# Kernel tuning notes

Hardware: AMD Instinct MI355X
Metric: run time of the kernel (lower is better)

The kernel has to match this reference:

```python
import jax, jax.numpy as jnp
import numpy as np

N_NODES = 100000
N_EDGES = 1600000
NODES_PER_GRAPH = 100  # equal-sized graphs -> batch = arange // 100
POOL_K = 30


def setup_inputs() -> dict:
    key = jax.random.key(0)
    ks = jax.random.split(key, 8)
    F_IN, H1, H2, OUT = 128, 128, 128, 64
    x = jax.random.normal(ks[0], (N_NODES, F_IN), dtype=jnp.float32)
    edge_index = jax.random.randint(ks[1], (2, N_EDGES), 0, N_NODES, dtype=jnp.int64)
    batch = (jnp.arange(N_NODES, dtype=jnp.int64) // NODES_PER_GRAPH)
    # Glorot-ish init for weights, zero bias (as PyG GCNConv defaults)
    W1 = jax.random.normal(ks[2], (F_IN, H1), dtype=jnp.float32) / np.sqrt(F_IN)
    b1 = jnp.zeros((H1,), dtype=jnp.float32)
    W2 = jax.random.normal(ks[3], (H1, H2), dtype=jnp.float32) / np.sqrt(H1)
    b2 = jnp.zeros((H2,), dtype=jnp.float32)
    W3 = jax.random.normal(ks[4], (H2, OUT), dtype=jnp.float32) / np.sqrt(H2)
    b3 = jnp.zeros((OUT,), dtype=jnp.float32)
    return {"x": x, "edge_index": edge_index, "batch": batch,
            "W1": W1, "b1": b1, "W2": W2, "b2": b2, "W3": W3, "b3": b3}


def _gcn_conv(x, src, dst, W, b):
    """PyG GCNConv: xW, add self-loops, symmetric D^-1/2 A D^-1/2 scatter-add, +bias."""
    n = x.shape[0]
    loops = jnp.arange(n, dtype=src.dtype)
    row = jnp.concatenate([src, loops])  # message source
    col = jnp.concatenate([dst, loops])  # aggregation target
    xw = x @ W
    deg = jax.ops.segment_sum(jnp.ones(col.shape[0], x.dtype), col, num_segments=n)
    dinv = jnp.where(deg > 0, jax.lax.rsqrt(deg), 0.0)
    norm = dinv[row] * dinv[col]  # [E+N]
    out = jax.ops.segment_sum(xw[row] * norm[:, None], col, num_segments=n)
    return out + b


def _sort_pool(x, k):
    """global_sort_pool: per-graph descending sort by last channel, take top-k, flatten.
    Graphs are equal-sized and contiguous, so reshape to [B, P, C]."""
    n, c = x.shape
    xb = x.reshape(n // NODES_PER_GRAPH, NODES_PER_GRAPH, c)  # [B, P, C]
    order = jnp.argsort(-xb[..., -1], axis=1)[:, :k]          # [B, k]
    topk = jnp.take_along_axis(xb, order[..., None], axis=1)  # [B, k, C]
    return topk.reshape(topk.shape[0], k * c)


def reference(x, edge_index, batch, W1, b1, W2, b2, W3, b3):
    src, dst = edge_index[0], edge_index[1]
    h = jax.nn.relu(_gcn_conv(x, src, dst, W1, b1))
    h = jax.nn.relu(_gcn_conv(h, src, dst, W2, b2))
    h = _gcn_conv(h, src, dst, W3, b3)
    return _sort_pool(h, POOL_K)
```

## Files before the change

kernel.cpp:

```cpp
#include <hip/hip_runtime.h>
#include <math.h>

static inline size_t ws_align(size_t x) { return (x + 255) & ~(size_t)255; }

__global__ void count_kernel(const int* __restrict__ dst, int* __restrict__ counts, int E) {
  int e = blockIdx.x * 256 + threadIdx.x;
  if (e < E) atomicAdd(&counts[dst[e]], 1);
}

__global__ __launch_bounds__(256) void scanA_kernel(const int* __restrict__ counts,
    int* __restrict__ bsums, int n) {
  __shared__ int red[4];
  const int base = blockIdx.x * 1024;
  const int tid = threadIdx.x;
  int s = 0;
  #pragma unroll
  for (int u = 0; u < 4; ++u) {
    int i = base + u * 256 + tid;
    s += (i < n) ? counts[i] : 0;
  }
  #pragma unroll
  for (int m = 1; m < 64; m <<= 1) s += __shfl_xor(s, m, 64);
  if ((tid & 63) == 0) red[tid >> 6] = s;
  __syncthreads();
  if (tid == 0) bsums[blockIdx.x] = red[0] + red[1] + red[2] + red[3];
}

__global__ __launch_bounds__(128) void scanB_kernel(int* __restrict__ bsums, int nb) {
  __shared__ int tmp[129];
  int tid = threadIdx.x;
  tmp[tid] = (tid < nb) ? bsums[tid] : 0;
  __syncthreads();
  if (tid == 0) {
    int run = 0;
    for (int i = 0; i < nb; ++i) { int v = tmp[i]; tmp[i] = run; run += v; }
  }
  __syncthreads();
  if (tid < nb) bsums[tid] = tmp[tid];
}

__global__ __launch_bounds__(1024) void scanC_kernel(const int* __restrict__ counts,
    const int* __restrict__ bsums, int* __restrict__ offsets, int* __restrict__ cursor,
    double* __restrict__ dinv, int n) {
  __shared__ int warpsums[16];
  const int tid = threadIdx.x;
  const int lane = tid & 63, wid = tid >> 6;
  const int i = blockIdx.x * 1024 + tid;
  int v = (i < n) ? counts[i] : 0;
  int x = v;
  #pragma unroll
  for (int d = 1; d < 64; d <<= 1) {
    int y = __shfl_up(x, d, 64);
    if (lane >= d) x += y;
  }
  if (lane == 63) warpsums[wid] = x;
  __syncthreads();
  if (wid == 0) {
    int w = (lane < 16) ? warpsums[lane] : 0;
    #pragma unroll
    for (int d = 1; d < 16; d <<= 1) {
      int y = __shfl_up(w, d, 64);
      if (lane >= d) w += y;
    }
    if (lane < 16) warpsums[lane] = w;
  }
  __syncthreads();
  int excl = bsums[blockIdx.x] + x - v + (wid > 0 ? warpsums[wid - 1] : 0);
  if (i < n) {
    offsets[i] = excl;
    cursor[i] = excl;
    dinv[i] = 1.0 / sqrt((double)(v + 1));
    if (i == n - 1) offsets[n] = excl + v;
  }
}

__global__ void scatter_kernel(const int* __restrict__ src, const int* __restrict__ dst,
    int* __restrict__ cursor, int* __restrict__ srcs, float* __restrict__ ew,
    const double* __restrict__ dinv, int E, int use_ew) {
  int e = blockIdx.x * 256 + threadIdx.x;
  if (e < E) {
    int s = src[e], d = dst[e];
    int p = atomicAdd(&cursor[d], 1);
    srcs[p] = s;
    if (use_ew) ew[p] = (float)(dinv[s] * dinv[d]);
  }
}

template<int H>
__global__ __launch_bounds__(512, 4) void gemm_kernel(const float* __restrict__ X,
    const float* __restrict__ W, float* __restrict__ out, int N) {
  __shared__ float xs[128 * 68];
  const int tid  = threadIdx.x;
  const int row0 = blockIdx.x * 64;
  #pragma unroll
  for (int p = 0; p < 4; ++p) {
    int idx = p * 512 + tid;
    int r  = idx & 63;
    int c4 = idx >> 6;
    int grow = row0 + r;
    float4 v = make_float4(0.f, 0.f, 0.f, 0.f);
    if (grow < N) v = *(const float4*)(X + (size_t)grow * 128 + c4 * 4);
    float vals[4] = {v.x, v.y, v.z, v.w};
    #pragma unroll
    for (int j = 0; j < 4; ++j)
      xs[(4 * c4 + j) * 68 + r] = vals[j];
  }
  __syncthreads();
  constexpr int CPT = H / 32;
  const int rowg = tid & 15;
  const int colg = tid >> 4;
  const float* wbase = W + colg * CPT;

  double acc[4][CPT];
  #pragma unroll
  for (int j = 0; j < 4; ++j)
    #pragma unroll
    for (int h = 0; h < CPT; ++h) acc[j][h] = 0.0;

  float4 aA = *(const float4*)(xs + 4 * rowg);
  float4 aB;
  float bA[CPT], bB[CPT];
  #pragma unroll
  for (int h = 0; h < CPT; ++h) bA[h] = wbase[h];

  #pragma unroll 1
  for (int k = 0; k < 128; k += 2) {
    aB = *(const float4*)(xs + (k + 1) * 68 + 4 * rowg);
    #pragma unroll
    for (int h = 0; h < CPT; ++h) bB[h] = wbase[(size_t)(k + 1) * H + h];
    {
      double a0 = (double)aA.x, a1 = (double)aA.y, a2 = (double)aA.z, a3 = (double)aA.w;
      double b[CPT];
      #pragma unroll
      for (int h = 0; h < CPT; ++h) b[h] = (double)bA[h];
      #pragma unroll
      for (int h = 0; h < CPT; ++h) {
        acc[0][h] = fma(a0, b[h], acc[0][h]);
        acc[1][h] = fma(a1, b[h], acc[1][h]);
        acc[2][h] = fma(a2, b[h], acc[2][h]);
        acc[3][h] = fma(a3, b[h], acc[3][h]);
      }
    }
    if (k + 2 < 128) {
      aA = *(const float4*)(xs + (k + 2) * 68 + 4 * rowg);
      #pragma unroll
      for (int h = 0; h < CPT; ++h) bA[h] = wbase[(size_t)(k + 2) * H + h];
    }
    {
      double a0 = (double)aB.x, a1 = (double)aB.y, a2 = (double)aB.z, a3 = (double)aB.w;
      double b[CPT];
      #pragma unroll
      for (int h = 0; h < CPT; ++h) b[h] = (double)bB[h];
      #pragma unroll
      for (int h = 0; h < CPT; ++h) {
        acc[0][h] = fma(a0, b[h], acc[0][h]);
        acc[1][h] = fma(a1, b[h], acc[1][h]);
        acc[2][h] = fma(a2, b[h], acc[2][h]);
        acc[3][h] = fma(a3, b[h], acc[3][h]);
      }
    }
  }
  #pragma unroll
  for (int j = 0; j < 4; ++j) {
    int grow = row0 + rowg * 4 + j;
    if (grow < N) {
      float* o = out + (size_t)grow * H + colg * CPT;
      if constexpr (CPT == 4) {
        float4 v = make_float4((float)acc[j][0], (float)acc[j][1],
                               (float)acc[j][2], (float)acc[j][3]);
        *(float4*)o = v;
      } else {
        float2 v = make_float2((float)acc[j][0], (float)acc[j][1]);
        *(float2*)o = v;
      }
    }
  }
}

template<int C, bool RELU, bool USE_EW>
__global__ __launch_bounds__(256) void gather_kernel(const float* __restrict__ xw,
    const double* __restrict__ dinv, const int* __restrict__ offs,
    const int* __restrict__ srcs, const float* __restrict__ ew,
    const float* __restrict__ bias, float* __restrict__ out, int N) {
  constexpr int LPR = C / 4;
  constexpr int EPI = 64 / LPR;
  constexpr int U = 8;
  const int node = blockIdx.x * 4 + (threadIdx.x >> 6);
  if (node >= N) return;
  const int lane = threadIdx.x & 63;
  const int grp  = lane / LPR;
  const int c0   = (lane % LPR) * 4;
  const int e0 = offs[node], e1 = offs[node + 1];
  const double di = dinv[node];
  double a0 = 0.0, a1 = 0.0, a2 = 0.0, a3 = 0.0;

  for (int base = e0; base < e1; base += U * EPI) {
    int ss[U];
    double ww[U];
    float4 vv[U];
    #pragma unroll
    for (int u = 0; u < U; ++u) {
      int ee = base + u * EPI + grp;
      int cl = ee < e1 ? ee : e1 - 1;
      ss[u] = srcs[cl];
      if (USE_EW) ww[u] = (double)ew[cl];
    }
    #pragma unroll
    for (int u = 0; u < U; ++u) {
      vv[u] = *(const float4*)(xw + (size_t)ss[u] * C + c0);
      if (!USE_EW) ww[u] = dinv[ss[u]];
    }
    #pragma unroll
    for (int u = 0; u < U; ++u) {
      int ee = base + u * EPI + grp;
      double w = (ee < e1) ? ww[u] : 0.0;
      a0 = fma(w, (double)vv[u].x, a0);
      a1 = fma(w, (double)vv[u].y, a1);
      a2 = fma(w, (double)vv[u].z, a2);
      a3 = fma(w, (double)vv[u].w, a3);
    }
  }
  #pragma unroll
  for (int m = LPR; m < 64; m <<= 1) {
    a0 += __shfl_xor(a0, m, 64);
    a1 += __shfl_xor(a1, m, 64);
    a2 += __shfl_xor(a2, m, 64);
    a3 += __shfl_xor(a3, m, 64);
  }
  if (grp == 0) {
    const double d2 = di * di;
    float4 sv = *(const float4*)(xw + (size_t)node * C + c0);
    float4 bv = *(const float4*)(bias + c0);
    double o0, o1, o2, o3;
    if (USE_EW) {
      o0 = a0 + fma(d2, (double)sv.x, (double)bv.x);
      o1 = a1 + fma(d2, (double)sv.y, (double)bv.y);
      o2 = a2 + fma(d2, (double)sv.z, (double)bv.z);
      o3 = a3 + fma(d2, (double)sv.w, (double)bv.w);
    } else {
      o0 = fma(di, a0, fma(d2, (double)sv.x, (double)bv.x));
      o1 = fma(di, a1, fma(d2, (double)sv.y, (double)bv.y));
      o2 = fma(di, a2, fma(d2, (double)sv.z, (double)bv.z));
      o3 = fma(di, a3, fma(d2, (double)sv.w, (double)bv.w));
    }
    if (RELU) {
      o0 = o0 > 0.0 ? o0 : 0.0; o1 = o1 > 0.0 ? o1 : 0.0;
      o2 = o2 > 0.0 ? o2 : 0.0; o3 = o3 > 0.0 ? o3 : 0.0;
    }
    *(float4*)(out + (size_t)node * C + c0) =
        make_float4((float)o0, (float)o1, (float)o2, (float)o3);
  }
}

__global__ __launch_bounds__(128) void sortpool_kernel(const float* __restrict__ h,
    float* __restrict__ out) {
  __shared__ float sv[128];
  __shared__ int si[128];
  int g = blockIdx.x;
  int tid = threadIdx.x;
  const float* hg = h + (size_t)g * 100 * 64;
  if (tid < 100) {
    sv[tid] = hg[tid * 64 + 63];
    si[tid] = tid;
  } else {
    sv[tid] = -3.0e38f;
    si[tid] = 1 << 30;
  }
  __syncthreads();
  for (int k = 2; k <= 128; k <<= 1) {
    for (int j = k >> 1; j > 0; j >>= 1) {
      int i = tid;
      int l = i ^ j;
      if (l > i) {
        float va = sv[i], vb = sv[l];
        int ia = si[i], ib = si[l];
        bool a_before_b = (va > vb) || (va == vb && ia < ib);
        bool up = ((i & k) == 0);
        bool sw = up ? !a_before_b : a_before_b;
        if (sw) { sv[i] = vb; sv[l] = va; si[i] = ib; si[l] = ia; }
      }
      __syncthreads();
    }
  }
  for (int t = tid; t < 30 * 64; t += 128) {
    int kk = t >> 6;
    int c = t & 63;
    out[(size_t)g * (30 * 64) + t] = hg[si[kk] * 64 + c];
  }
}

extern "C" void kernel_launch(void* const* d_in, const int* in_sizes, int n_in,
                              void* d_out, int out_size, void* d_ws, size_t ws_size,
                              hipStream_t stream) {
  const float* x  = (const float*)d_in[0];
  const int*   ei = (const int*)d_in[1];
  const float* W1 = (const float*)d_in[3];
  const float* b1 = (const float*)d_in[4];
  const float* W2 = (const float*)d_in[5];
  const float* b2 = (const float*)d_in[6];
  const float* W3 = (const float*)d_in[7];
  const float* b3 = (const float*)d_in[8];

  const int N = in_sizes[0] / 128;
  const int E = in_sizes[1] / 2;
  const int* src = ei;
  const int* dst = ei + E;
  (void)n_in; (void)out_size;

  const int nb = (N + 1023) / 1024;

  char* ws = (char*)d_ws;
  size_t off = 0;
  auto alloc = [&](size_t bytes) { char* p = ws + off; off = ws_align(off + bytes); return p; };
  float*  xw      = (float*) alloc((size_t)N * 128 * 4);
  float*  h       = (float*) alloc((size_t)N * 128 * 4);
  double* dinv    = (double*)alloc((size_t)N * 8);
  int*    offsets = (int*)   alloc(((size_t)N + 1) * 4);
  int*    cursor  = (int*)   alloc((size_t)N * 4);
  int*    counts  = (int*)   alloc((size_t)N * 4);
  int*    srcs    = (int*)   alloc((size_t)E * 4);
  int*    bsums   = (int*)   alloc((size_t)(nb + 1) * 4);
  float*  ew      = (float*) alloc((size_t)E * 4);
  const bool use_ew = (off <= ws_size);

  hipMemsetAsync(counts, 0, (size_t)N * 4, stream);
  count_kernel<<<(E + 255) / 256, 256, 0, stream>>>(dst, counts, E);
  scanA_kernel<<<nb, 256, 0, stream>>>(counts, bsums, N);
  scanB_kernel<<<1, 128, 0, stream>>>(bsums, nb);
  scanC_kernel<<<nb, 1024, 0, stream>>>(counts, bsums, offsets, cursor, dinv, N);
  scatter_kernel<<<(E + 255) / 256, 256, 0, stream>>>(src, dst, cursor, srcs, ew, dinv, E, use_ew ? 1 : 0);

  const int gblocks  = (N + 63) / 64;
  const int nblocks4 = (N + 3) / 4;

  gemm_kernel<128><<<gblocks, 512, 0, stream>>>(x, W1, xw, N);
  if (use_ew) {
    gather_kernel<128, true,  true><<<nblocks4, 256, 0, stream>>>(xw, dinv, offsets, srcs, ew, b1, h, N);
    gemm_kernel<128><<<gblocks, 512, 0, stream>>>(h, W2, xw, N);
    gather_kernel<128, true,  true><<<nblocks4, 256, 0, stream>>>(xw, dinv, offsets, srcs, ew, b2, h, N);
    gemm_kernel<64 ><<<gblocks, 512, 0, stream>>>(h, W3, xw, N);
    gather_kernel<64,  false, true><<<nblocks4, 256, 0, stream>>>(xw, dinv, offsets, srcs, ew, b3, h, N);
  } else {
    gather_kernel<128, true,  false><<<nblocks4, 256, 0, stream>>>(xw, dinv, offsets, srcs, ew, b1, h, N);
    gemm_kernel<128><<<gblocks, 512, 0, stream>>>(h, W2, xw, N);
    gather_kernel<128, true,  false><<<nblocks4, 256, 0, stream>>>(xw, dinv, offsets, srcs, ew, b2, h, N);
    gemm_kernel<64 ><<<gblocks, 512, 0, stream>>>(h, W3, xw, N);
    gather_kernel<64,  false, false><<<nblocks4, 256, 0, stream>>>(xw, dinv, offsets, srcs, ew, b3, h, N);
  }
  sortpool_kernel<<<N / 100, 128, 0, stream>>>(h, (float*)d_out);
}
```

Baseline: 883.0 us.

## Fuse aggregation with next-layer GEMM and final gather with sort-pool

Each layer's neighbor aggregation, bias and ReLU now write a 64-node tile into shared memory, and the next layer's weight GEMM runs on that tile in the same kernel, so the intermediate h never goes through global memory. The last aggregation is fused with sort pooling: each block handles one graph, keeps the 100x64 result in shared memory, sorts it, and emits the top-k rows directly. This removes several launches and global round trips. In exchange, the fused kernels use large shared-memory footprints and fewer waves per node during the gather, so occupancy and latency hiding for the irregular gathers may drop.

```diff
diff --git a/kernel.cpp b/kernel.cpp
--- a/kernel.cpp
+++ b/kernel.cpp
@@ -166,127 +166,254 @@
     if (grow < N) {
       float* o = out + (size_t)grow * H + colg * CPT;
       if constexpr (CPT == 4) {
-        float4 v = make_float4((float)acc[j][0], (float)acc[j][1],
-                               (float)acc[j][2], (float)acc[j][3]);
-        *(float4*)o = v;
+        *(float4*)o = make_float4((float)acc[j][0], (float)acc[j][1],
+                                  (float)acc[j][2], (float)acc[j][3]);
       } else {
-        float2 v = make_float2((float)acc[j][0], (float)acc[j][1]);
-        *(float2*)o = v;
-      }
-    }
-  }
-}
-
-template<int C, bool RELU, bool USE_EW>
-__global__ __launch_bounds__(256) void gather_kernel(const float* __restrict__ xw,
+        *(float2*)o = make_float2((float)acc[j][0], (float)acc[j][1]);
+      }
+    }
+  }
+}
+
+template<int HOUT, bool USE_EW>
+__global__ __launch_bounds__(512, 4) void fused_kernel(const float* __restrict__ xw_in,
+    const double* __restrict__ dinv, const int* __restrict__ offs,
+    const int* __restrict__ srcs, const float* __restrict__ ew,
+    const float* __restrict__ bias, const float* __restrict__ Wn,
+    float* __restrict__ xw_out, int N) {
+  __shared__ float xs[128 * 68];
+  const int tid  = threadIdx.x;
+  const int wave = tid >> 6, lane = tid & 63;
+  const int row0 = blockIdx.x * 64;
+  const int grp  = lane >> 5;
+  const int c0   = (lane & 31) * 4;
+
+  for (int i = 0; i < 8; ++i) {
+    const int n_loc = wave * 8 + i;
+    const int node = row0 + n_loc;
+    if (node >= N) break;
+    const int e0 = offs[node], e1 = offs[node + 1];
+    const double di = dinv[node];
+    double a0 = 0.0, a1 = 0.0, a2 = 0.0, a3 = 0.0;
+    for (int base = e0; base < e1; base += 16) {
+      int ss[8]; double ww[8]; float4 vv[8];
+      #pragma unroll
+      for (int u = 0; u < 8; ++u) {
+        int ee = base + u * 2 + grp;
+        int cl = ee < e1 ? ee : e1 - 1;
+        ss[u] = srcs[cl];
+        if (USE_EW) ww[u] = (double)ew[cl];
+      }
+      #pragma unroll
+      for (int u = 0; u < 8; ++u) {
+        vv[u] = *(const float4*)(xw_in + (size_t)ss[u] * 128 + c0);
+        if (!USE_EW) ww[u] = dinv[ss[u]];
+      }
+      #pragma unroll
+      for (int u = 0; u < 8; ++u) {
+        int ee = base + u * 2 + grp;
+        double w = (ee < e1) ? ww[u] : 0.0;
+        a0 = fma(w, (double)vv[u].x, a0);
+        a1 = fma(w, (double)vv[u].y, a1);
+        a2 = fma(w, (double)vv[u].z, a2);
+        a3 = fma(w, (double)vv[u].w, a3);
+      }
+    }
+    a0 += __shfl_xor(a0, 32, 64);
+    a1 += __shfl_xor(a1, 32, 64);
+    a2 += __shfl_xor(a2, 32, 64);
+    a3 += __shfl_xor(a3, 32, 64);
+    if (grp == 0) {
+      const double d2 = di * di;
+      float4 sv = *(const float4*)(xw_in + (size_t)node * 128 + c0);
+      float4 bv = *(const float4*)(bias + c0);
+      double o0, o1, o2, o3;
+      if (USE_EW) {
+        o0 = a0 + fma(d2, (double)sv.x, (double)bv.x);
+        o1 = a1 + fma(d2, (double)sv.y, (double)bv.y);
+        o2 = a2 + fma(d2, (double)sv.z, (double)bv.z);
+        o3 = a3 + fma(d2, (double)sv.w, (double)bv.w);
+      } else {
+        o0 = fma(di, a0, fma(d2, (double)sv.x, (double)bv.x));
+        o1 = fma(di, a1, fma(d2, (double)sv.y, (double)bv.y));
+        o2 = fma(di, a2, fma(d2, (double)sv.z, (double)bv.z));
+        o3 = fma(di, a3, fma(d2, (double)sv.w, (double)bv.w));
+      }
+      o0 = o0 > 0.0 ? o0 : 0.0; o1 = o1 > 0.0 ? o1 : 0.0;
+      o2 = o2 > 0.0 ? o2 : 0.0; o3 = o3 > 0.0 ? o3 : 0.0;
+      xs[(c0 + 0) * 68 + n_loc] = (float)o0;
+      xs[(c0 + 1) * 68 + n_loc] = (float)o1;
+      xs[(c0 + 2) * 68 + n_loc] = (float)o2;
+      xs[(c0 + 3) * 68 + n_loc] = (float)o3;
+    }
+  }
+  __syncthreads();
+
+  constexpr int CPT = HOUT / 32;
+  const int rowg = tid & 15;
+  const int colg = tid >> 4;
+  const float* wbase = Wn + colg * CPT;
+
+  double acc[4][CPT];
+  #pragma unroll
+  for (int j = 0; j < 4; ++j)
+    #pragma unroll
+    for (int h = 0; h < CPT; ++h) acc[j][h] = 0.0;
+
+  float4 aA = *(const float4*)(xs + 4 * rowg);
+  float4 aB;
+  float bA[CPT], bB[CPT];
+  #pragma unroll
+  for (int h = 0; h < CPT; ++h) bA[h] = wbase[h];
+
+  #pragma unroll 1
+  for (int k = 0; k < 128; k += 2) {
+    aB = *(const float4*)(xs + (k + 1) * 68 + 4 * rowg);
+    #pragma unroll
+    for (int h = 0; h < CPT; ++h) bB[h] = wbase[(size_t)(k + 1) * HOUT + h];
+    {
+      double a0 = (double)aA.x, a1 = (double)aA.y, a2 = (double)aA.z, a3 = (double)aA.w;
+      double b[CPT];
+      #pragma unroll
+      for (int h = 0; h < CPT; ++h) b[h] = (double)bA[h];
+      #pragma unroll
+      for (int h = 0; h < CPT; ++h) {
+        acc[0][h] = fma(a0, b[h], acc[0][h]);
+        acc[1][h] = fma(a1, b[h], acc[1][h]);
+        acc[2][h] = fma(a2, b[h], acc[2][h]);
+        acc[3][h] = fma(a3, b[h], acc[3][h]);
+      }
+    }
+    if (k + 2 < 128) {
+      aA = *(const float4*)(xs + (k + 2) * 68 + 4 * rowg);
+      #pragma unroll
+      for (int h = 0; h < CPT; ++h) bA[h] = wbase[(size_t)(k + 2) * HOUT + h];
+    }
+    {
+      double a0 = (double)aB.x, a1 = (double)aB.y, a2 = (double)aB.z, a3 = (double)aB.w;
+      double b[CPT];
+      #pragma unroll
+      for (int h = 0; h < CPT; ++h) b[h] = (double)bB[h];
+      #pragma unroll
+      for (int h = 0; h < CPT; ++h) {
+        acc[0][h] = fma(a0, b[h], acc[0][h]);
+        acc[1][h] = fma(a1, b[h], acc[1][h]);
+        acc[2][h] = fma(a2, b[h], acc[2][h]);
+        acc[3][h] = fma(a3, b[h], acc[3][h]);
+      }
+    }
+  }
+  #pragma unroll
+  for (int j = 0; j < 4; ++j) {
+    int grow = row0 + rowg * 4 + j;
+    if (grow < N) {
+      float* o = xw_out + (size_t)grow * HOUT + colg * CPT;
+      if constexpr (CPT == 4) {
+        *(float4*)o = make_float4((float)acc[j][0], (float)acc[j][1],
+                                  (float)acc[j][2], (float)acc[j][3]);
+      } else {
+        *(float2*)o = make_float2((float)acc[j][0], (float)acc[j][1]);
+      }
+    }
+  }
+}
+
+template<bool USE_EW>
+__global__ __launch_bounds__(512, 2) void gather_pool_kernel(const float* __restrict__ xw,
     const double* __restrict__ dinv, const int* __restrict__ offs,
     const int* __restrict__ srcs, const float* __restrict__ ew,
     const float* __restrict__ bias, float* __restrict__ out, int N) {
-  constexpr int LPR = C / 4;
-  constexpr int EPI = 64 / LPR;
-  constexpr int U = 8;
-  const int node = blockIdx.x * 4 + (threadIdx.x >> 6);
-  if (node >= N) return;
-  const int lane = threadIdx.x & 63;
-  const int grp  = lane / LPR;
-  const int c0   = (lane % LPR) * 4;
-  const int e0 = offs[node], e1 = offs[node + 1];
-  const double di = dinv[node];
-  double a0 = 0.0, a1 = 0.0, a2 = 0.0, a3 = 0.0;
-
-  for (int base = e0; base < e1; base += U * EPI) {
-    int ss[U];
-    double ww[U];
-    float4 vv[U];
-    #pragma unroll
-    for (int u = 0; u < U; ++u) {
-      int ee = base + u * EPI + grp;
-      int cl = ee < e1 ? ee : e1 - 1;
-      ss[u] = srcs[cl];
-      if (USE_EW) ww[u] = (double)ew[cl];
-    }
-    #pragma unroll
-    for (int u = 0; u < U; ++u) {
-      vv[u] = *(const float4*)(xw + (size_t)ss[u] * C + c0);
-      if (!USE_EW) ww[u] = dinv[ss[u]];
-    }
-    #pragma unroll
-    for (int u = 0; u < U; ++u) {
-      int ee = base + u * EPI + grp;
-      double w = (ee < e1) ? ww[u] : 0.0;
-      a0 = fma(w, (double)vv[u].x, a0);
-      a1 = fma(w, (double)vv[u].y, a1);
-      a2 = fma(w, (double)vv[u].z, a2);
-      a3 = fma(w, (double)vv[u].w, a3);
-    }
-  }
-  #pragma unroll
-  for (int m = LPR; m < 64; m <<= 1) {
-    a0 += __shfl_xor(a0, m, 64);
-    a1 += __shfl_xor(a1, m, 64);
-    a2 += __shfl_xor(a2, m, 64);
-    a3 += __shfl_xor(a3, m, 64);
-  }
-  if (grp == 0) {
-    const double d2 = di * di;
-    float4 sv = *(const float4*)(xw + (size_t)node * C + c0);
-    float4 bv = *(const float4*)(bias + c0);
-    double o0, o1, o2, o3;
-    if (USE_EW) {
-      o0 = a0 + fma(d2, (double)sv.x, (double)bv.x);
-      o1 = a1 + fma(d2, (double)sv.y, (double)bv.y);
-      o2 = a2 + fma(d2, (double)sv.z, (double)bv.z);
-      o3 = a3 + fma(d2, (double)sv.w, (double)bv.w);
-    } else {
-      o0 = fma(di, a0, fma(d2, (double)sv.x, (double)bv.x));
-      o1 = fma(di, a1, fma(d2, (double)sv.y, (double)bv.y));
-      o2 = fma(di, a2, fma(d2, (double)sv.z, (double)bv.z));
-      o3 = fma(di, a3, fma(d2, (double)sv.w, (double)bv.w));
-    }
-    if (RELU) {
-      o0 = o0 > 0.0 ? o0 : 0.0; o1 = o1 > 0.0 ? o1 : 0.0;
-      o2 = o2 > 0.0 ? o2 : 0.0; o3 = o3 > 0.0 ? o3 : 0.0;
-    }
-    *(float4*)(out + (size_t)node * C + c0) =
-        make_float4((float)o0, (float)o1, (float)o2, (float)o3);
-  }
-}
-
-__global__ __launch_bounds__(128) void sortpool_kernel(const float* __restrict__ h,
-    float* __restrict__ out) {
+  __shared__ float hl[100 * 64];
   __shared__ float sv[128];
   __shared__ int si[128];
-  int g = blockIdx.x;
-  int tid = threadIdx.x;
-  const float* hg = h + (size_t)g * 100 * 64;
-  if (tid < 100) {
-    sv[tid] = hg[tid * 64 + 63];
-    si[tid] = tid;
-  } else {
-    sv[tid] = -3.0e38f;
-    si[tid] = 1 << 30;
+  const int tid  = threadIdx.x;
+  const int wave = tid >> 6, lane = tid & 63;
+  const int g = blockIdx.x;
+  const int grp = lane >> 4;
+  const int c0  = (lane & 15) * 4;
+
+  for (int n_loc = wave; n_loc < 100; n_loc += 8) {
+    const int node = g * 100 + n_loc;
+    const int e0 = offs[node], e1 = offs[node + 1];
+    const double di = dinv[node];
+    double a0 = 0.0, a1 = 0.0, a2 = 0.0, a3 = 0.0;
+    for (int base = e0; base < e1; base += 16) {
+      int ss[4]; double ww[4]; float4 vv[4];
+      #pragma unroll
+      for (int u = 0; u < 4; ++u) {
+        int ee = base + u * 4 + grp;
+        int cl = ee < e1 ? ee : e1 - 1;
+        ss[u] = srcs[cl];
+        if (USE_EW) ww[u] = (double)ew[cl];
+      }
+      #pragma unroll
+      for (int u = 0; u < 4; ++u) {
+        vv[u] = *(const float4*)(xw + (size_t)ss[u] * 64 + c0);
+        if (!USE_EW) ww[u] = dinv[ss[u]];
+      }
+      #pragma unroll
+      for (int u = 0; u < 4; ++u) {
+        int ee = base + u * 4 + grp;
+        double w = (ee < e1) ? ww[u] : 0.0;
+        a0 = fma(w, (double)vv[u].x, a0);
+        a1 = fma(w, (double)vv[u].y, a1);
+        a2 = fma(w, (double)vv[u].z, a2);
+        a3 = fma(w, (double)vv[u].w, a3);
+      }
+    }
+    #pragma unroll
+    for (int m = 16; m < 64; m <<= 1) {
+      a0 += __shfl_xor(a0, m, 64);
+      a1 += __shfl_xor(a1, m, 64);
+      a2 += __shfl_xor(a2, m, 64);
+      a3 += __shfl_xor(a3, m, 64);
+    }
+    if (grp == 0) {
+      const double d2 = di * di;
+      float4 svf = *(const float4*)(xw + (size_t)node * 64 + c0);
+      float4 bv  = *(const float4*)(bias + c0);
+      double o0, o1, o2, o3;
+      if (USE_EW) {
+        o0 = a0 + fma(d2, (double)svf.x, (double)bv.x);
+        o1 = a1 + fma(d2, (double)svf.y, (double)bv.y);
+        o2 = a2 + fma(d2, (double)svf.z, (double)bv.z);
+        o3 = a3 + fma(d2, (double)svf.w, (double)bv.w);
+      } else {
+        o0 = fma(di, a0, fma(d2, (double)svf.x, (double)bv.x));
+        o1 = fma(di, a1, fma(d2, (double)svf.y, (double)bv.y));
+        o2 = fma(di, a2, fma(d2, (double)svf.z, (double)bv.z));
+        o3 = fma(di, a3, fma(d2, (double)svf.w, (double)bv.w));
+      }
+      hl[n_loc * 64 + c0 + 0] = (float)o0;
+      hl[n_loc * 64 + c0 + 1] = (float)o1;
+      hl[n_loc * 64 + c0 + 2] = (float)o2;
+      hl[n_loc * 64 + c0 + 3] = (float)o3;
+    }
+  }
+  __syncthreads();
+  if (tid < 128) {
+    if (tid < 100) { sv[tid] = hl[tid * 64 + 63]; si[tid] = tid; }
+    else           { sv[tid] = -3.0e38f;          si[tid] = 1 << 30; }
   }
   __syncthreads();
   for (int k = 2; k <= 128; k <<= 1) {
     for (int j = k >> 1; j > 0; j >>= 1) {
-      int i = tid;
-      int l = i ^ j;
-      if (l > i) {
-        float va = sv[i], vb = sv[l];
-        int ia = si[i], ib = si[l];
-        bool a_before_b = (va > vb) || (va == vb && ia < ib);
-        bool up = ((i & k) == 0);
-        bool sw = up ? !a_before_b : a_before_b;
-        if (sw) { sv[i] = vb; sv[l] = va; si[i] = ib; si[l] = ia; }
+      if (tid < 128) {
+        int l = tid ^ j;
+        if (l > tid) {
+          float va = sv[tid], vb = sv[l];
+          int ia = si[tid], ib = si[l];
+          bool a_before_b = (va > vb) || (va == vb && ia < ib);
+          bool up = ((tid & k) == 0);
+          bool sw = up ? !a_before_b : a_before_b;
+          if (sw) { sv[tid] = vb; sv[l] = va; si[tid] = ib; si[l] = ia; }
+        }
       }
       __syncthreads();
     }
   }
-  for (int t = tid; t < 30 * 64; t += 128) {
-    int kk = t >> 6;
-    int c = t & 63;
-    out[(size_t)g * (30 * 64) + t] = hg[si[kk] * 64 + c];
-  }
+  for (int t = tid; t < 30 * 64; t += 512)
+    out[(size_t)g * (30 * 64) + t] = hl[si[t >> 6] * 64 + (t & 63)];
 }
 
 extern "C" void kernel_launch(void* const* d_in, const int* in_sizes, int n_in,
@@ -330,22 +457,16 @@
   scanC_kernel<<<nb, 1024, 0, stream>>>(counts, bsums, offsets, cursor, dinv, N);
   scatter_kernel<<<(E + 255) / 256, 256, 0, stream>>>(src, dst, cursor, srcs, ew, dinv, E, use_ew ? 1 : 0);
 
-  const int gblocks  = (N + 63) / 64;
-  const int nblocks4 = (N + 3) / 4;
+  const int gblocks = (N + 63) / 64;
 
   gemm_kernel<128><<<gblocks, 512, 0, stream>>>(x, W1, xw, N);
   if (use_ew) {
-    gather_kernel<128, true,  true><<<nblocks4, 256, 0, stream>>>(xw, dinv, offsets, srcs, ew, b1, h, N);
-    gemm_kernel<128><<<gblocks, 512, 0, stream>>>(h, W2, xw, N);
-    gather_kernel<128, true,  true><<<nblocks4, 256, 0, stream>>>(xw, dinv, offsets, srcs, ew, b2, h, N);
-    gemm_kernel<64 ><<<gblocks, 512, 0, stream>>>(h, W3, xw, N);
-    gather_kernel<64,  false, true><<<nblocks4, 256, 0, stream>>>(xw, dinv, offsets, srcs, ew, b3, h, N);
+    fused_kernel<128, true ><<<gblocks, 512, 0, stream>>>(xw, dinv, offsets, srcs, ew, b1, W2, h, N);
+    fused_kernel<64,  true ><<<gblocks, 512, 0, stream>>>(h,  dinv, offsets, srcs, ew, b2, W3, xw, N);
+    gather_pool_kernel<true ><<<N / 100, 512, 0, stream>>>(xw, dinv, offsets, srcs, ew, b3, (float*)d_out, N);
   } else {
-    gather_kernel<128, true,  false><<<nblocks4, 256, 0, stream>>>(xw, dinv, offsets, srcs, ew, b1, h, N);
-    gemm_kernel<128><<<gblocks, 512, 0, stream>>>(h, W2, xw, N);
-    gather_kernel<128, true,  false><<<nblocks4, 256, 0, stream>>>(xw, dinv, offsets, srcs, ew, b2, h, N);
-    gemm_kernel<64 ><<<gblocks, 512, 0, stream>>>(h, W3, xw, N);
-    gather_kernel<64,  false, false><<<nblocks4, 256, 0, stream>>>(xw, dinv, offsets, srcs, ew, b3, h, N);
-  }
-  sortpool_kernel<<<N / 100, 128, 0, stream>>>(h, (float*)d_out);
-}
+    fused_kernel<128, false><<<gblocks, 512, 0, stream>>>(xw, dinv, offsets, srcs, ew, b1, W2, h, N);
+    fused_kernel<64,  false><<<gblocks, 512, 0, stream>>>(h,  dinv, offsets, srcs, ew, b2, W3, xw, N);
+    gather_pool_kernel<false><<<N / 100, 512, 0, stream>>>(xw, dinv, offsets, srcs, ew, b3, (float*)d_out, N);
+  }
+}
```

Measured after the change: 847.2 us. -4.1%, faster.
